# Performance work log

Hardware: AMD Instinct MI355X
Metric: run time of the kernel (lower is better)

The kernel has to match this reference:

```python
import jax, jax.numpy as jnp
import numpy as np

N = 100000
E = 1600000
IN_DIM, HID, OUT = 512, 128, 16


def setup_inputs() -> dict:
    key = jax.random.key(0)
    ks = jax.random.split(key, 8)
    x = jax.random.normal(ks[0], (N, IN_DIM), dtype=jnp.float32)
    edge_index = jax.random.randint(ks[1], (2, E), 0, N, dtype=jnp.int64)
    # GCNConv params (Glorot-ish scale) and Linear head
    W1 = jax.random.normal(ks[2], (IN_DIM, HID), dtype=jnp.float32) / np.sqrt(IN_DIM)
    b1 = jnp.zeros((HID,), dtype=jnp.float32)
    W2 = jax.random.normal(ks[3], (HID, HID), dtype=jnp.float32) / np.sqrt(HID)
    b2 = jnp.zeros((HID,), dtype=jnp.float32)
    Wl = jax.random.normal(ks[4], (HID, OUT), dtype=jnp.float32) / np.sqrt(HID)
    bl = jnp.zeros((OUT,), dtype=jnp.float32)
    return {"x": x, "edge_index": edge_index, "W1": W1, "b1": b1,
            "W2": W2, "b2": b2, "Wl": Wl, "bl": bl}


def _gcn_conv(x, W, b, src, dst, deg_inv_sqrt, deg_inv):
    # h = x @ W ; out[dst] += norm * h[src]; self-loop adds h[i]/deg[i]
    h = x @ W                                           # [N, D]
    norm = deg_inv_sqrt[src] * deg_inv_sqrt[dst]        # [E]
    msgs = h[src] * norm[:, None]                       # [E, D] gather
    agg = jax.ops.segment_sum(msgs, dst, num_segments=x.shape[0])  # scatter
    agg = agg + h * deg_inv[:, None]                    # self-loop term
    return agg + b


def reference(x, edge_index, W1, b1, W2, b2, Wl, bl):
    src, dst = edge_index[0], edge_index[1]
    n = x.shape[0]
    ones = jnp.ones(src.shape[0], dtype=x.dtype)
    # degree with self-loops (PyG gcn_norm counts in-degree at target + 1)
    deg = jax.ops.segment_sum(ones, dst, num_segments=n) + 1.0
    deg_inv_sqrt = jax.lax.rsqrt(deg)
    deg_inv = 1.0 / deg

    h = _gcn_conv(x, W1, b1, src, dst, deg_inv_sqrt, deg_inv)
    h = jax.nn.relu(h)
    # dropout: inference mode (training=False) -> identity
    h = _gcn_conv(h, W2, b2, src, dst, deg_inv_sqrt, deg_inv)
    embeddings = jax.nn.relu(h)
    out = embeddings @ Wl + bl
    return out, embeddings
```

## Files before the change

### kernel.cpp

```cpp
#include <hip/hip_runtime.h>

#define NN 100000
#define EE 1600000
#define IND 512
#define HIDD 128
#define OUTD 16
#define DEG_BLKS 128
#define GEMM_BLKS 1563

typedef __bf16 bf16x8 __attribute__((ext_vector_type(8)));
typedef float f32x4 __attribute__((ext_vector_type(4)));

__device__ __forceinline__ ushort f2bf(float f) {
    union { float f; uint u; } v; v.f = f;
    uint r = v.u + 0x7FFFu + ((v.u >> 16) & 1u);
    return (ushort)(r >> 16);
}

__global__ void k_prep(const float* __restrict__ W1, const float* __restrict__ W2,
                       ushort* __restrict__ Wt1, ushort* __restrict__ Wt2) {
    int b = blockIdx.x, tid = threadIdx.x;
    if (b < 256) {
        int i = b * 256 + tid;
        int k = i >> 7, n = i & 127;
        Wt1[n * 512 + k] = f2bf(W1[i]);
    } else {
        int i = (b - 256) * 256 + tid;
        int k = i >> 7, n = i & 127;
        Wt2[n * 128 + k] = f2bf(W2[i]);
    }
}

__global__ void k_scan_local(const int* __restrict__ deg, int* __restrict__ incl,
                             int* __restrict__ bsum) {
    __shared__ int s[256];
    int tid = threadIdx.x;
    int i = blockIdx.x * 256 + tid;
    int v = (i < NN) ? deg[i] : 0;
    s[tid] = v;
    __syncthreads();
    for (int off = 1; off < 256; off <<= 1) {
        int t = (tid >= off) ? s[tid - off] : 0;
        __syncthreads();
        s[tid] += t;
        __syncthreads();
    }
    if (i < NN) incl[i] = s[tid];
    if (tid == 255) bsum[blockIdx.x] = s[255];
}

__global__ void k_scan_bsum(const int* __restrict__ bsum, int* __restrict__ boff, int n) {
    __shared__ int s[512];
    int tid = threadIdx.x;
    int v = (tid < n) ? bsum[tid] : 0;
    s[tid] = v;
    __syncthreads();
    for (int off = 1; off < 512; off <<= 1) {
        int t = (tid >= off) ? s[tid - off] : 0;
        __syncthreads();
        s[tid] += t;
        __syncthreads();
    }
    if (tid < n) boff[tid] = s[tid] - v;
}

__global__ void k_scan_final(const int* __restrict__ incl, const int* __restrict__ deg,
                             const int* __restrict__ boff, int* __restrict__ rs,
                             int* __restrict__ cursor, float* __restrict__ dis,
                             float* __restrict__ dinv) {
    int i = blockIdx.x * 256 + threadIdx.x;
    if (i < NN) {
        int d = deg[i];
        int v = incl[i] + boff[i >> 8];
        int start = v - d;
        rs[i] = start;
        cursor[i] = start;
        if (i == NN - 1) rs[NN] = v;
        float df = (float)(d + 1);
        dis[i] = rsqrtf(df);
        dinv[i] = 1.0f / df;
    }
}

__global__ void k_fill(const int* __restrict__ src, const int* __restrict__ dst,
                       const float* __restrict__ dis, int* __restrict__ cursor,
                       int2* __restrict__ ew) {
    int i = blockIdx.x * blockDim.x + threadIdx.x;
    int stride = gridDim.x * blockDim.x;
    for (; i < EE; i += stride) {
        int d = dst[i];
        int s = src[i];
        int pos = atomicAdd(&cursor[d], 1);
        ew[pos] = make_int2(s, __float_as_int(dis[s] * dis[d]));
    }
}

template <int K, bool AFP32>
__device__ __forceinline__ void gemm_body(const void* __restrict__ Ap,
                                          const ushort* __restrict__ Wt,
                                          ushort* __restrict__ C, int M, int blk) {
    __shared__ ushort As[64][40];
    __shared__ ushort Ws[128][40];
    int tid = threadIdx.x;
    int row0 = blk * 64;
    int wid = tid >> 6, lane = tid & 63;
    int wm = (wid & 1) * 32, wn = (wid >> 1) * 64;
    int lm = lane & 15, lk8 = (lane >> 4) * 8;

    f32x4 acc[4][2];
#pragma unroll
    for (int q = 0; q < 4; q++)
#pragma unroll
        for (int r = 0; r < 2; r++) acc[q][r] = (f32x4){0.f, 0.f, 0.f, 0.f};

    int arow = tid >> 2, akg = tid & 3;
    int gr = row0 + arow;

    for (int k0 = 0; k0 < K; k0 += 32) {
        if (AFP32) {
            const float* A = (const float*)Ap;
            float4 v0 = make_float4(0.f, 0.f, 0.f, 0.f), v1 = v0;
            if (gr < M) {
                const float* p = A + (size_t)gr * K + k0 + akg * 8;
                v0 = *(const float4*)(p);
                v1 = *(const float4*)(p + 4);
            }
            uint4 pk;
            pk.x = (uint)f2bf(v0.x) | ((uint)f2bf(v0.y) << 16);
            pk.y = (uint)f2bf(v0.z) | ((uint)f2bf(v0.w) << 16);
            pk.z = (uint)f2bf(v1.x) | ((uint)f2bf(v1.y) << 16);
            pk.w = (uint)f2bf(v1.z) | ((uint)f2bf(v1.w) << 16);
            *(uint4*)&As[arow][akg * 8] = pk;
        } else {
            const ushort* A = (const ushort*)Ap;
            uint4 v = make_uint4(0, 0, 0, 0);
            if (gr < M) v = *(const uint4*)(A + (size_t)gr * K + k0 + akg * 8);
            *(uint4*)&As[arow][akg * 8] = v;
        }
#pragma unroll
        for (int p = 0; p < 2; p++) {
            int idx = p * 256 + tid;
            int n = idx >> 2, kg = idx & 3;
            uint4 v = *(const uint4*)(Wt + (size_t)n * K + k0 + kg * 8);
            *(uint4*)&Ws[n][kg * 8] = v;
        }
        __syncthreads();

        bf16x8 xf[2], wf[4];
#pragma unroll
        for (int r = 0; r < 2; r++) xf[r] = *(const bf16x8*)&As[wm + r * 16 + lm][lk8];
#pragma unroll
        for (int q = 0; q < 4; q++) wf[q] = *(const bf16x8*)&Ws[wn + q * 16 + lm][lk8];
#pragma unroll
        for (int q = 0; q < 4; q++)
#pragma unroll
            for (int r = 0; r < 2; r++)
                acc[q][r] = __builtin_amdgcn_mfma_f32_16x16x32_bf16(wf[q], xf[r], acc[q][r], 0, 0, 0);
        __syncthreads();
    }

    int cn4 = (lane >> 4) * 4;
#pragma unroll
    for (int r = 0; r < 2; r++) {
        int m = row0 + wm + r * 16 + lm;
        if (m < M) {
#pragma unroll
            for (int q = 0; q < 4; q++) {
                int n = wn + q * 16 + cn4;
                uint2 o;
                o.x = (uint)f2bf(acc[q][r][0]) | ((uint)f2bf(acc[q][r][1]) << 16);
                o.y = (uint)f2bf(acc[q][r][2]) | ((uint)f2bf(acc[q][r][3]) << 16);
                *(uint2*)(C + (size_t)m * 128 + n) = o;
            }
        }
    }
}

__global__ __launch_bounds__(256) void k_mega1(const float* __restrict__ x,
                                               const ushort* __restrict__ Wt1,
                                               ushort* __restrict__ C,
                                               const int* __restrict__ dst,
                                               int* __restrict__ deg) {
    if (blockIdx.x < DEG_BLKS) {
        int i = blockIdx.x * 256 + threadIdx.x;
        int stride = DEG_BLKS * 256;
        for (; i < EE; i += stride) atomicAdd(&deg[dst[i]], 1);
    } else {
        gemm_body<IND, true>(x, Wt1, C, NN, blockIdx.x - DEG_BLKS);
    }
}

__global__ __launch_bounds__(256) void k_gemm2(const ushort* __restrict__ A,
                                               const ushort* __restrict__ Wt,
                                               ushort* __restrict__ C) {
    gemm_body<HIDD, false>(A, Wt, C, NN, blockIdx.x);
}

template <bool HEAD>
__global__ __launch_bounds__(256) void k_agg_bf(const ushort* __restrict__ h,
                                                const int* __restrict__ rs,
                                                const int2* __restrict__ ew,
                                                const float* __restrict__ dinv,
                                                const float* __restrict__ bias,
                                                void* __restrict__ yv,
                                                const float* __restrict__ Wl,
                                                const float* __restrict__ bl,
                                                float* __restrict__ outp) {
    __shared__ float wl_s[HEAD ? 128 * 17 : 1];
    int tid = threadIdx.x;
    int lane = tid & 63;
    if (HEAD) {
        for (int i = tid; i < 2048; i += 256) wl_s[(i >> 4) * 17 + (i & 15)] = Wl[i];
        __syncthreads();
    }
    const uint* h32 = (const uint*)h;
    float b0 = bias[lane * 2], b1 = bias[lane * 2 + 1];

    for (int node = blockIdx.x * 4 + (tid >> 6); node < NN; node += gridDim.x * 4) {
        float dv = dinv[node];
        uint sv = h32[(size_t)node * 64 + lane];
        float acc0 = __uint_as_float(sv << 16) * dv;
        float acc1 = __uint_as_float(sv & 0xffff0000u) * dv;
        int e  = __builtin_amdgcn_readfirstlane(rs[node]);
        int e1 = __builtin_amdgcn_readfirstlane(rs[node + 1]);

#define EL(i) int2 p##i = ew[e + i]; uint g##i = h32[(size_t)(uint)p##i.x * 64 + lane];
#define EA(i) { float w##i = __int_as_float(p##i.y); \
    acc0 += w##i * __uint_as_float(g##i << 16); \
    acc1 += w##i * __uint_as_float(g##i & 0xffff0000u); }

        for (; e + 16 <= e1; e += 16) {
            EL(0) EL(1) EL(2) EL(3) EL(4) EL(5) EL(6) EL(7)
            EL(8) EL(9) EL(10) EL(11) EL(12) EL(13) EL(14) EL(15)
            EA(0) EA(1) EA(2) EA(3) EA(4) EA(5) EA(6) EA(7)
            EA(8) EA(9) EA(10) EA(11) EA(12) EA(13) EA(14) EA(15)
        }
        for (; e + 4 <= e1; e += 4) {
            EL(0) EL(1) EL(2) EL(3)
            EA(0) EA(1) EA(2) EA(3)
        }
        for (; e < e1; ++e) {
            EL(0)
            EA(0)
        }
#undef EL
#undef EA

        acc0 = fmaxf(acc0 + b0, 0.0f);
        acc1 = fmaxf(acc1 + b1, 0.0f);

        if (!HEAD) {
            ((uint*)yv)[(size_t)node * 64 + lane] =
                (uint)f2bf(acc0) | ((uint)f2bf(acc1) << 16);
        } else {
            ((float2*)yv)[(size_t)node * 64 + lane] = make_float2(acc0, acc1);
            float part[16];
#pragma unroll
            for (int o = 0; o < 16; o++)
                part[o] = acc0 * wl_s[(lane * 2) * 17 + o] + acc1 * wl_s[(lane * 2 + 1) * 17 + o];
#pragma unroll
            for (int s = 1; s < 64; s <<= 1) {
#pragma unroll
                for (int o = 0; o < 16; o++) part[o] += __shfl_xor(part[o], s, 64);
            }
            if (lane == 0) {
                float* op = outp + (size_t)node * 16;
                *(float4*)(op + 0)  = make_float4(part[0] + bl[0], part[1] + bl[1], part[2] + bl[2], part[3] + bl[3]);
                *(float4*)(op + 4)  = make_float4(part[4] + bl[4], part[5] + bl[5], part[6] + bl[6], part[7] + bl[7]);
                *(float4*)(op + 8)  = make_float4(part[8] + bl[8], part[9] + bl[9], part[10] + bl[10], part[11] + bl[11]);
                *(float4*)(op + 12) = make_float4(part[12] + bl[12], part[13] + bl[13], part[14] + bl[14], part[15] + bl[15]);
            }
        }
    }
}

extern "C" void kernel_launch(void* const* d_in, const int* in_sizes, int n_in,
                              void* d_out, int out_size, void* d_ws, size_t ws_size,
                              hipStream_t stream) {
    const float* x  = (const float*)d_in[0];
    const int* ei   = (const int*)d_in[1];
    const float* W1 = (const float*)d_in[2];
    const float* b1 = (const float*)d_in[3];
    const float* W2 = (const float*)d_in[4];
    const float* b2 = (const float*)d_in[5];
    const float* Wl = (const float*)d_in[6];
    const float* bl = (const float*)d_in[7];
    const int* src = ei;
    const int* dst = ei + EE;

    float* outp = (float*)d_out;
    float* emb  = outp + (size_t)NN * OUTD;

    int2* ew    = (int2*)d_ws;
    ushort* h_a = (ushort*)(ew + EE);
    ushort* h_b = h_a + (size_t)NN * 128;
    ushort* Wt1 = h_b + (size_t)NN * 128;
    ushort* Wt2 = Wt1 + 128 * 512;
    int* deg    = (int*)(Wt2 + 128 * 128);
    float* dis  = (float*)(deg + NN);
    float* dinv = dis + NN;
    int* incl   = (int*)(dinv + NN);
    int* rs     = incl + NN;
    int* cursor = rs + NN + 8;
    int* bsum   = cursor + NN;
    int* boff   = bsum + 512;

    const int NB_N = (NN + 255) / 256;

    hipMemsetAsync(deg, 0, (size_t)NN * sizeof(int), stream);
    k_prep<<<320, 256, 0, stream>>>(W1, W2, Wt1, Wt2);
    k_mega1<<<DEG_BLKS + GEMM_BLKS, 256, 0, stream>>>(x, Wt1, h_a, dst, deg);
    k_scan_local<<<NB_N, 256, 0, stream>>>(deg, incl, bsum);
    k_scan_bsum<<<1, 512, 0, stream>>>(bsum, boff, NB_N);
    k_scan_final<<<NB_N, 256, 0, stream>>>(incl, deg, boff, rs, cursor, dis, dinv);
    k_fill<<<2048, 256, 0, stream>>>(src, dst, dis, cursor, ew);

    k_agg_bf<false><<<2048, 256, 0, stream>>>(h_a, rs, ew, dinv, b1, h_b,
                                              nullptr, nullptr, nullptr);
    k_gemm2<<<GEMM_BLKS, 256, 0, stream>>>(h_b, Wt2, h_a);
    k_agg_bf<true><<<2048, 256, 0, stream>>>(h_a, rs, ew, dinv, b2, emb,
                                             Wl, bl, outp);
}
```

Measured before the change: 392.0 us.

## Split aggregation wavefront into two half-waves per node and separate output head

Each aggregation wavefront now splits into two 32-lane halves. Each half handles alternate edges and loads 8-byte bf16x4 feature chunks, and the halves combine with a cross-half shuffle. The grid-stride loop is replaced by one node per wavefront, launching one block per four nodes. The fused linear head, with its 16-output shuffle reduction, moves into a separate k_out kernel that rereads the fp32 embeddings. This is meant to raise memory-level parallelism in the gather and remove the heavy shuffle tail, at the cost of an extra launch and an extra read of the embeddings.

```diff
diff --git a/kernel.cpp b/kernel.cpp
--- a/kernel.cpp
+++ b/kernel.cpp
@@ -196,82 +196,111 @@
     gemm_body<HIDD, false>(A, Wt, C, NN, blockIdx.x);
 }
 
-template <bool HEAD>
-__global__ __launch_bounds__(256) void k_agg_bf(const ushort* __restrict__ h,
-                                                const int* __restrict__ rs,
-                                                const int2* __restrict__ ew,
-                                                const float* __restrict__ dinv,
-                                                const float* __restrict__ bias,
-                                                void* __restrict__ yv,
-                                                const float* __restrict__ Wl,
-                                                const float* __restrict__ bl,
-                                                float* __restrict__ outp) {
-    __shared__ float wl_s[HEAD ? 128 * 17 : 1];
-    int tid = threadIdx.x;
-    int lane = tid & 63;
-    if (HEAD) {
-        for (int i = tid; i < 2048; i += 256) wl_s[(i >> 4) * 17 + (i & 15)] = Wl[i];
-        __syncthreads();
-    }
-    const uint* h32 = (const uint*)h;
-    float b0 = bias[lane * 2], b1 = bias[lane * 2 + 1];
-
-    for (int node = blockIdx.x * 4 + (tid >> 6); node < NN; node += gridDim.x * 4) {
+template <bool OUTF32>
+__global__ __launch_bounds__(256) void k_agg(const ushort* __restrict__ h,
+                                             const int* __restrict__ rs,
+                                             const int2* __restrict__ ew,
+                                             const float* __restrict__ dinv,
+                                             const float* __restrict__ bias,
+                                             void* __restrict__ yv) {
+    int node = blockIdx.x * 4 + (threadIdx.x >> 6);
+    int lane = threadIdx.x & 63;
+    if (node >= NN) return;
+    int half = lane >> 5, c = lane & 31;
+    const uint2* h64 = (const uint2*)h;
+
+    float acc0 = 0.f, acc1 = 0.f, acc2 = 0.f, acc3 = 0.f;
+    if (half == 0) {
         float dv = dinv[node];
-        uint sv = h32[(size_t)node * 64 + lane];
-        float acc0 = __uint_as_float(sv << 16) * dv;
-        float acc1 = __uint_as_float(sv & 0xffff0000u) * dv;
-        int e  = __builtin_amdgcn_readfirstlane(rs[node]);
-        int e1 = __builtin_amdgcn_readfirstlane(rs[node + 1]);
-
-#define EL(i) int2 p##i = ew[e + i]; uint g##i = h32[(size_t)(uint)p##i.x * 64 + lane];
+        uint2 sv = h64[(size_t)node * 32 + c];
+        acc0 = __uint_as_float(sv.x << 16) * dv;
+        acc1 = __uint_as_float(sv.x & 0xffff0000u) * dv;
+        acc2 = __uint_as_float(sv.y << 16) * dv;
+        acc3 = __uint_as_float(sv.y & 0xffff0000u) * dv;
+    }
+
+    int e = rs[node], e1 = rs[node + 1];
+
+#define EL(i) int2 p##i = ew[e + 2 * i + half]; \
+              uint2 g##i = h64[(size_t)(uint)p##i.x * 32 + c];
 #define EA(i) { float w##i = __int_as_float(p##i.y); \
-    acc0 += w##i * __uint_as_float(g##i << 16); \
-    acc1 += w##i * __uint_as_float(g##i & 0xffff0000u); }
-
-        for (; e + 16 <= e1; e += 16) {
-            EL(0) EL(1) EL(2) EL(3) EL(4) EL(5) EL(6) EL(7)
-            EL(8) EL(9) EL(10) EL(11) EL(12) EL(13) EL(14) EL(15)
-            EA(0) EA(1) EA(2) EA(3) EA(4) EA(5) EA(6) EA(7)
-            EA(8) EA(9) EA(10) EA(11) EA(12) EA(13) EA(14) EA(15)
-        }
-        for (; e + 4 <= e1; e += 4) {
-            EL(0) EL(1) EL(2) EL(3)
-            EA(0) EA(1) EA(2) EA(3)
-        }
-        for (; e < e1; ++e) {
-            EL(0)
-            EA(0)
-        }
+    acc0 += w##i * __uint_as_float(g##i.x << 16); \
+    acc1 += w##i * __uint_as_float(g##i.x & 0xffff0000u); \
+    acc2 += w##i * __uint_as_float(g##i.y << 16); \
+    acc3 += w##i * __uint_as_float(g##i.y & 0xffff0000u); }
+
+    for (; e + 16 <= e1; e += 16) {
+        EL(0) EL(1) EL(2) EL(3) EL(4) EL(5) EL(6) EL(7)
+        EA(0) EA(1) EA(2) EA(3) EA(4) EA(5) EA(6) EA(7)
+    }
+    for (; e + 4 <= e1; e += 4) {
+        EL(0) EL(1)
+        EA(0) EA(1)
+    }
+    if (e + 2 <= e1) {
+        EL(0)
+        EA(0)
+        e += 2;
+    }
+    if (e < e1 && half == 0) {
+        int2 p = ew[e];
+        uint2 g = h64[(size_t)(uint)p.x * 32 + c];
+        float w = __int_as_float(p.y);
+        acc0 += w * __uint_as_float(g.x << 16);
+        acc1 += w * __uint_as_float(g.x & 0xffff0000u);
+        acc2 += w * __uint_as_float(g.y << 16);
+        acc3 += w * __uint_as_float(g.y & 0xffff0000u);
+    }
 #undef EL
 #undef EA
 
-        acc0 = fmaxf(acc0 + b0, 0.0f);
-        acc1 = fmaxf(acc1 + b1, 0.0f);
-
-        if (!HEAD) {
-            ((uint*)yv)[(size_t)node * 64 + lane] =
-                (uint)f2bf(acc0) | ((uint)f2bf(acc1) << 16);
+    acc0 += __shfl_xor(acc0, 32, 64);
+    acc1 += __shfl_xor(acc1, 32, 64);
+    acc2 += __shfl_xor(acc2, 32, 64);
+    acc3 += __shfl_xor(acc3, 32, 64);
+
+    if (half == 0) {
+        float4 bv = *(const float4*)(bias + c * 4);
+        acc0 = fmaxf(acc0 + bv.x, 0.f);
+        acc1 = fmaxf(acc1 + bv.y, 0.f);
+        acc2 = fmaxf(acc2 + bv.z, 0.f);
+        acc3 = fmaxf(acc3 + bv.w, 0.f);
+        if (OUTF32) {
+            *(float4*)((float*)yv + (size_t)node * 128 + c * 4) =
+                make_float4(acc0, acc1, acc2, acc3);
         } else {
-            ((float2*)yv)[(size_t)node * 64 + lane] = make_float2(acc0, acc1);
-            float part[16];
-#pragma unroll
-            for (int o = 0; o < 16; o++)
-                part[o] = acc0 * wl_s[(lane * 2) * 17 + o] + acc1 * wl_s[(lane * 2 + 1) * 17 + o];
-#pragma unroll
-            for (int s = 1; s < 64; s <<= 1) {
-#pragma unroll
-                for (int o = 0; o < 16; o++) part[o] += __shfl_xor(part[o], s, 64);
-            }
-            if (lane == 0) {
-                float* op = outp + (size_t)node * 16;
-                *(float4*)(op + 0)  = make_float4(part[0] + bl[0], part[1] + bl[1], part[2] + bl[2], part[3] + bl[3]);
-                *(float4*)(op + 4)  = make_float4(part[4] + bl[4], part[5] + bl[5], part[6] + bl[6], part[7] + bl[7]);
-                *(float4*)(op + 8)  = make_float4(part[8] + bl[8], part[9] + bl[9], part[10] + bl[10], part[11] + bl[11]);
-                *(float4*)(op + 12) = make_float4(part[12] + bl[12], part[13] + bl[13], part[14] + bl[14], part[15] + bl[15]);
-            }
+            uint2 o;
+            o.x = (uint)f2bf(acc0) | ((uint)f2bf(acc1) << 16);
+            o.y = (uint)f2bf(acc2) | ((uint)f2bf(acc3) << 16);
+            *(uint2*)((ushort*)yv + (size_t)node * 128 + c * 4) = o;
         }
     }
+}
+
+__global__ __launch_bounds__(256) void k_out(const float* __restrict__ emb,
+                                             const float* __restrict__ Wl,
+                                             const float* __restrict__ bl,
+                                             float* __restrict__ out) {
+    __shared__ float wl_s[128 * 16];
+    __shared__ float es[16][129];
+    int tid = threadIdx.x;
+    int row0 = blockIdx.x * 16;
+#pragma unroll
+    for (int p = 0; p < 8; p++) wl_s[p * 256 + tid] = Wl[p * 256 + tid];
+#pragma unroll
+    for (int p = 0; p < 8; p++) {
+        int idx = p * 256 + tid;
+        int r = idx >> 7, c = idx & 127;
+        int gr = row0 + r;
+        es[r][c] = (gr < NN) ? emb[(size_t)gr * 128 + c] : 0.0f;
+    }
+    __syncthreads();
+    int r = tid >> 4, o = tid & 15;
+    float acc = bl[o];
+#pragma unroll
+    for (int k = 0; k < 128; k++) acc += es[r][k] * wl_s[k * 16 + o];
+    int gr = row0 + r;
+    if (gr < NN) out[(size_t)gr * 16 + o] = acc;
 }
 
 extern "C" void kernel_launch(void* const* d_in, const int* in_sizes, int n_in,
@@ -315,9 +344,8 @@
     k_scan_final<<<NB_N, 256, 0, stream>>>(incl, deg, boff, rs, cursor, dis, dinv);
     k_fill<<<2048, 256, 0, stream>>>(src, dst, dis, cursor, ew);
 
-    k_agg_bf<false><<<2048, 256, 0, stream>>>(h_a, rs, ew, dinv, b1, h_b,
-                                              nullptr, nullptr, nullptr);
+    k_agg<false><<<(NN + 3) / 4, 256, 0, stream>>>(h_a, rs, ew, dinv, b1, h_b);
     k_gemm2<<<GEMM_BLKS, 256, 0, stream>>>(h_b, Wt2, h_a);
-    k_agg_bf<true><<<2048, 256, 0, stream>>>(h_a, rs, ew, dinv, b2, emb,
-                                             Wl, bl, outp);
-}
+    k_agg<true><<<(NN + 3) / 4, 256, 0, stream>>>(h_a, rs, ew, dinv, b2, emb);
+    k_out<<<(NN + 15) / 16, 256, 0, stream>>>(emb, Wl, bl, outp);
+}
```

After: 383.0 us. 2.3% less time.
